# Kernel tuning notes

Measured on AMD Instinct MI355X. Metric: run time of the kernel, lower is better.

Reference implementation:

```python
import jax, jax.numpy as jnp
import numpy as np

L, B, N, D, H, DH, M = 2, 8, 1024, 256, 4, 64, 512
EPS = 1e-5


def setup_inputs() -> dict:
    key = jax.random.key(0)
    ks = jax.random.split(key, 24)
    n = lambda k, shape, s=0.02: jax.random.normal(k, shape, dtype=jnp.float32) * s
    return {
        "x": jax.random.normal(ks[0], (B, N, D), dtype=jnp.float32),
        "ln1_g": jnp.ones((L, D), jnp.float32), "ln1_b": jnp.zeros((L, D), jnp.float32),
        "w_qkv": n(ks[1], (L, D, 3 * H * DH)),
        "w_out": n(ks[2], (L, H * DH, D)), "b_out": jnp.zeros((L, D), jnp.float32),
        "ln2_g": jnp.ones((L, D), jnp.float32), "ln2_b": jnp.zeros((L, D), jnp.float32),
        "w_fc1": n(ks[3], (L, D, M)), "b_fc1": jnp.zeros((L, M), jnp.float32),
        "wh": n(ks[4], (L, M, 3), 0.3), "bh": jnp.zeros((L, M), jnp.float32),
        "wv": n(ks[5], (L, M, 3), 0.3), "bv": jnp.zeros((L, M), jnp.float32),
        "bn_g": jnp.ones((L, M), jnp.float32), "bn_b": jnp.zeros((L, M), jnp.float32),
        "bn_m": n(ks[6], (L, M), 0.1),
        "bn_v": jax.random.uniform(ks[7], (L, M), jnp.float32, 0.5, 1.5),
        "w_fc2": n(ks[8], (L, M, D)), "b_fc2": jnp.zeros((L, D), jnp.float32),
        "ls_w1": n(ks[9], (L, D, D // 4)), "ls_w2": n(ks[10], (L, D // 4, D)),
    }


def _ln(z, g, b):
    mu = z.mean(-1, keepdims=True)
    var = ((z - mu) ** 2).mean(-1, keepdims=True)
    return (z - mu) / jnp.sqrt(var + EPS) * g + b


def _lsrc(z, w1, w2):
    # SE gate: global mean over tokens -> FC -> ReLU -> FC -> sigmoid -> scale
    s = jax.nn.sigmoid(jax.nn.relu(z.mean(1) @ w1) @ w2)  # [B, D]
    return z * s[:, None, :]


def reference(x, ln1_g, ln1_b, w_qkv, w_out, b_out, ln2_g, ln2_b, w_fc1, b_fc1,
              wh, bh, wv, bv, bn_g, bn_b, bn_m, bn_v, w_fc2, b_fc2, ls_w1, ls_w2):
    scale = DH ** -0.5
    for l in range(L):
        # --- MHSA (pre-LN) ---
        h = _ln(x, ln1_g[l], ln1_b[l])
        qkv = h @ w_qkv[l]                                  # [B,N,3*H*DH]
        q, k, v = jnp.split(qkv, 3, axis=-1)
        split = lambda t: t.reshape(B, N, H, DH).transpose(0, 2, 1, 3)  # [B,H,N,DH]
        q, k, v = split(q), split(k), split(v)
        attn = jax.nn.softmax(jnp.einsum('bhid,bhjd->bhij', q, k) * scale, axis=-1)
        o = jnp.einsum('bhij,bhjd->bhid', attn, v)
        o = o.transpose(0, 2, 1, 3).reshape(B, N, H * DH)
        y = o @ w_out[l] + b_out[l]                          # dropout = identity (eval)
        x = _lsrc(x + y, ls_w1[l], ls_w2[l])
        # --- MLP with ACB depthwise conv over the token axis ---
        y = jax.nn.gelu(_ln(x, ln2_g[l], ln2_b[l]) @ w_fc1[l] + b_fc1[l], approximate=False)
        # conv_h: depthwise 1x3 conv along N (zero pad)
        yp = jnp.pad(y, ((0, 0), (1, 1), (0, 0)))
        ch = wh[l, :, 0] * yp[:, :-2] + wh[l, :, 1] * yp[:, 1:-1] + wh[l, :, 2] * yp[:, 2:] + bh[l]
        # conv_v: 3x1 depthwise conv on height-1 input with pad 1 -> only center tap
        cv = wv[l, :, 1] * y + bv[l]
        z = ch + cv
        z = (z - bn_m[l]) / jnp.sqrt(bn_v[l] + EPS) * bn_g[l] + bn_b[l]  # BN (eval)
        z = jax.nn.gelu(z, approximate=False)
        y = z @ w_fc2[l] + b_fc2[l]
        x = _lsrc(x + y, ls_w1[l], ls_w2[l])
    return x
```

## Files before the change

kernel.cpp:

```cpp
#include <hip/hip_runtime.h>
#include <hip/hip_bf16.h>
#include <math.h>

#define EPSF 1e-5f

typedef short bf16x8 __attribute__((ext_vector_type(8)));
typedef float f32x4  __attribute__((ext_vector_type(4)));

#define S_BARRIER   __asm__ volatile("s_barrier" ::: "memory")
#define S_WAITV(n)  __asm__ volatile("s_waitcnt vmcnt(" #n ")" ::: "memory")
#define S_WAITL0    __asm__ volatile("s_waitcnt lgkmcnt(0)" ::: "memory")

__device__ __forceinline__ float gelu_f(float z){
  return 0.5f*z*(1.0f + erff(z*0.70710678118654752f));
}
__device__ __forceinline__ unsigned short f2bf(float f){
  unsigned u = __float_as_uint(f);
  u += 0x7FFFu + ((u >> 16) & 1u);
  return (unsigned short)(u >> 16);
}
__device__ __forceinline__ float bf2f(unsigned short u){
  return __uint_as_float((unsigned)u << 16);
}
__device__ __forceinline__ void gll16(const unsigned short* g, unsigned short* l){
  __builtin_amdgcn_global_load_lds(
    (const __attribute__((address_space(1))) unsigned int*)g,
    (__attribute__((address_space(3))) unsigned int*)l, 16, 0, 0);
}

__global__ void tcast_all_k(const float* __restrict__ wqkv, const float* __restrict__ wout,
                            const float* __restrict__ wfc1, const float* __restrict__ wfc2,
                            unsigned short* __restrict__ oqkv, unsigned short* __restrict__ oout,
                            unsigned short* __restrict__ ofc1, unsigned short* __restrict__ ofc2,
                            const float* __restrict__ wh, const float* __restrict__ bh,
                            const float* __restrict__ wv, const float* __restrict__ bv,
                            const float* __restrict__ g, const float* __restrict__ bb,
                            const float* __restrict__ mm, const float* __restrict__ vv,
                            float* __restrict__ cp){
  int idx = blockIdx.x*256 + threadIdx.x;
  if (idx < 1048576){
    int l = idx >> 19; int r = idx & 524287;
    const float* in; unsigned short* out; int K, N, base;
    if (r < 196608)      { in=wqkv+ (long)l*196608; out=oqkv+(long)l*196608; K=256; N=768; base=r; }
    else if (r < 262144) { in=wout+ (long)l*65536;  out=oout+(long)l*65536;  K=256; N=256; base=r-196608; }
    else if (r < 393216) { in=wfc1+ (long)l*131072; out=ofc1+(long)l*131072; K=256; N=512; base=r-262144; }
    else                 { in=wfc2+ (long)l*131072; out=ofc2+(long)l*131072; K=512; N=256; base=r-393216; }
    int n = base / K, k = base % K;
    out[base] = f2bf(in[(long)k*N + n]);
  } else if (idx < 1048576 + 1024){
    int j2 = idx - 1048576;
    int l = j2 >> 9, j = j2 & 511;
    int o = l*512 + j;
    float sc = g[o]*rsqrtf(vv[o] + EPSF);
    float* c = cp + (long)l*6*512;
    c[0*512+j] = wh[o*3+0];
    c[1*512+j] = wh[o*3+1] + wv[o*3+1];
    c[2*512+j] = wh[o*3+2];
    c[3*512+j] = bh[o] + bv[o];
    c[4*512+j] = sc;
    c[5*512+j] = bb[o] - mm[o]*sc;
  }
}

__global__ void ln_bf_k(const float* __restrict__ x, const float* __restrict__ g,
                        const float* __restrict__ b, unsigned short* __restrict__ out){
  const int wv = threadIdx.x >> 6, lane = threadIdx.x & 63;
  const int row = blockIdx.x*4 + wv;
  const int c4 = lane*4;
  float4 v = *reinterpret_cast<const float4*>(x + (long)row*256 + c4);
  float s  = v.x+v.y+v.z+v.w;
  float s2 = v.x*v.x+v.y*v.y+v.z*v.z+v.w*v.w;
  #pragma unroll
  for (int o=32;o>0;o>>=1){ s += __shfl_xor(s,o); s2 += __shfl_xor(s2,o); }
  const float mu = s*(1.f/256.f);
  const float rstd = rsqrtf(s2*(1.f/256.f) - mu*mu + EPSF);
  float4 gg = *reinterpret_cast<const float4*>(g + c4);
  float4 bb = *reinterpret_cast<const float4*>(b + c4);
  ushort4 u;
  u.x = f2bf((v.x-mu)*rstd*gg.x + bb.x);
  u.y = f2bf((v.y-mu)*rstd*gg.y + bb.y);
  u.z = f2bf((v.z-mu)*rstd*gg.z + bb.z);
  u.w = f2bf((v.w-mu)*rstd*gg.w + bb.w);
  *reinterpret_cast<ushort4*>(out + (long)row*256 + c4) = u;
}

__global__ void seapply_ln_k(float* __restrict__ x, const float* __restrict__ gate,
                             const float* __restrict__ g, const float* __restrict__ b,
                             unsigned short* __restrict__ out){
  const int wv = threadIdx.x >> 6, lane = threadIdx.x & 63;
  const int row = blockIdx.x*4 + wv;
  const int bi = row >> 10;
  const int c4 = lane*4;
  float4 v = *reinterpret_cast<const float4*>(x + (long)row*256 + c4);
  float4 gt = *reinterpret_cast<const float4*>(gate + bi*256 + c4);
  v.x*=gt.x; v.y*=gt.y; v.z*=gt.z; v.w*=gt.w;
  *reinterpret_cast<float4*>(x + (long)row*256 + c4) = v;
  float s  = v.x+v.y+v.z+v.w;
  float s2 = v.x*v.x+v.y*v.y+v.z*v.z+v.w*v.w;
  #pragma unroll
  for (int o=32;o>0;o>>=1){ s += __shfl_xor(s,o); s2 += __shfl_xor(s2,o); }
  const float mu = s*(1.f/256.f);
  const float rstd = rsqrtf(s2*(1.f/256.f) - mu*mu + EPSF);
  float4 gg = *reinterpret_cast<const float4*>(g + c4);
  float4 bb = *reinterpret_cast<const float4*>(b + c4);
  ushort4 u;
  u.x = f2bf((v.x-mu)*rstd*gg.x + bb.x);
  u.y = f2bf((v.y-mu)*rstd*gg.y + bb.y);
  u.z = f2bf((v.z-mu)*rstd*gg.z + bb.z);
  u.w = f2bf((v.w-mu)*rstd*gg.w + bb.w);
  *reinterpret_cast<ushort4*>(out + (long)row*256 + c4) = u;
}

__global__ void seapply_out_k(const float* __restrict__ x, const float* __restrict__ gate,
                              float* __restrict__ o){
  long o4 = ((long)blockIdx.x*256 + threadIdx.x)*4;
  float4 v = *reinterpret_cast<const float4*>(x+o4);
  float4 g = *reinterpret_cast<const float4*>(gate + (((o4>>18)<<8) | (o4 & 255)));
  v.x*=g.x; v.y*=g.y; v.z*=g.z; v.w*=g.w;
  *reinterpret_cast<float4*>(o+o4) = v;
}

template<int ACT, bool RES, bool BIAS, int OUT, int BMT, int BNT, bool CS>
__global__ __launch_bounds__(256,2)
void gmm_k(const unsigned short* __restrict__ A,
           const unsigned short* __restrict__ Bt,
           void* __restrict__ Cv, int ldc,
           const float* __restrict__ bias,
           const float* __restrict__ res,
           int K, unsigned short* __restrict__ vtb,
           float* __restrict__ cm)
{
  __shared__ unsigned short As[2][BMT*64];
  __shared__ unsigned short Bs[2][BNT*64];
  float* C = (float*)Cv;
  unsigned short* Cb = (unsigned short*)Cv;
  const int tid  = threadIdx.x;
  const int wave = tid>>6, lane = tid&63;
  constexpr int NI = BMT/32;
  constexpr int NJ = BNT/32;
  constexpr int NDMA = BMT/32 + BNT/32;
  const int wm = (wave>>1)*(16*NI), wn = (wave&1)*(BNT/2);
  const int m0 = blockIdx.y*BMT, n0 = blockIdx.x*BNT;
  const int lrow = lane&15, quad = lane>>4;

  f32x4 acc[NI][NJ];
  #pragma unroll
  for (int i=0;i<NI;i++)
    #pragma unroll
    for (int j=0;j<NJ;j++)
      #pragma unroll
      for (int r=0;r<4;r++) acc[i][j][r]=0.f;

  auto stage = [&](int kt, int buf){
    const int k0 = kt<<6;
    #pragma unroll
    for (int it2=0; it2<BMT/32; it2++){
      int idx = tid + it2*256;
      int row = idx>>3, c = idx&7;
      gll16(A + (long)(m0+row)*K + k0 + c*8, &As[buf][idx*8]);
    }
    #pragma unroll
    for (int it2=0; it2<BNT/32; it2++){
      int idx = tid + it2*256;
      int row = idx>>3, c = idx&7;
      gll16(Bt + (long)(n0+row)*K + k0 + c*8, &Bs[buf][idx*8]);
    }
  };

  const int iters = K >> 6;
  stage(0, 0);

  for (int it=0; it<iters; it++){
    const int cur = it & 1;
    if (it+1 < iters){
      stage(it+1, cur^1);
      if constexpr (NDMA==8) { S_WAITV(8); }
      else if constexpr (NDMA==6) { S_WAITV(6); }
      else { S_WAITV(4); }
    } else {
      S_WAITV(0);
    }
    S_BARRIER;

    #pragma unroll
    for (int s=0;s<2;s++){
      bf16x8 a[NI], b[NJ];
      const int ck = s*4 + quad;
      #pragma unroll
      for (int i=0;i<NI;i++)
        a[i] = *reinterpret_cast<const bf16x8*>(&As[cur][(wm+16*i+lrow)*64 + ck*8]);
      #pragma unroll
      for (int j=0;j<NJ;j++)
        b[j] = *reinterpret_cast<const bf16x8*>(&Bs[cur][(wn+16*j+lrow)*64 + ck*8]);
      #pragma unroll
      for (int i=0;i<NI;i++)
        #pragma unroll
        for (int j=0;j<NJ;j++)
          acc[i][j] = __builtin_amdgcn_mfma_f32_16x16x32_bf16(a[i], b[j], acc[i][j], 0,0,0);
    }
    S_WAITL0;
    S_BARRIER;
  }

  if constexpr (OUT==2){
    if (n0 >= 512){
      unsigned short* lt = (unsigned short*)&As[0][0];
      #pragma unroll
      for (int i=0;i<NI;i++){
        const int row_l0 = wm + 16*i + quad*4;
        #pragma unroll
        for (int j=0;j<NJ;j++){
          const int col_l = wn + 16*j + lrow;
          #pragma unroll
          for (int r=0;r<4;r++){
            const int row_l = row_l0 + r;
            lt[col_l*128 + (((row_l>>3) ^ (col_l&7))<<3) + (row_l&7)] = f2bf(acc[i][j][r]);
          }
        }
      }
      __syncthreads();
      const int bb = m0 >> 10, nn0 = m0 & 1023;
      #pragma unroll
      for (int it2=0; it2<8; it2++){
        int idx = tid + it2*256;
        int col_l = idx >> 4;
        int row8 = (idx & 15) << 3;
        uint4 v = *reinterpret_cast<const uint4*>(&lt[col_l*128 + (((row8>>3) ^ (col_l&7))<<3)]);
        int col = n0 + col_l;
        int h = (col-512) >> 6, d = (col-512) & 63;
        *reinterpret_cast<uint4*>(&vtb[(long)((bb*4+h)*64 + d)*1024 + nn0 + row8]) = v;
      }
      return;
    }
    #pragma unroll
    for (int i=0;i<NI;i++){
      const int row0 = m0 + wm + 16*i + quad*4;
      #pragma unroll
      for (int j=0;j<NJ;j++){
        const int col = n0 + wn + 16*j + lrow;
        #pragma unroll
        for (int r=0;r<4;r++)
          Cb[(long)(row0+r)*512 + col] = f2bf(acc[i][j][r]);
      }
    }
    return;
  }

  float csum[NJ];
  #pragma unroll
  for (int j=0;j<NJ;j++) csum[j] = 0.f;

  #pragma unroll
  for (int i=0;i<NI;i++){
    const int row0 = m0 + wm + 16*i + quad*4;
    #pragma unroll
    for (int j=0;j<NJ;j++){
      const int col = n0 + wn + 16*j + lrow;
      const float bv = BIAS ? bias[col] : 0.f;
      #pragma unroll
      for (int r=0;r<4;r++){
        const long off = (long)(row0+r)*ldc + col;
        float v = acc[i][j][r] + bv;
        if (RES) v += res[off];
        if (ACT==1) v = gelu_f(v);
        if (CS) csum[j] += v;
        if (OUT==1) Cb[off] = f2bf(v); else C[off] = v;
      }
    }
  }
  if (CS){
    float* red = (float*)&As[0][0];
    for (int j = tid; j < BNT; j += 256) red[j] = 0.f;
    __syncthreads();
    #pragma unroll
    for (int j=0;j<NJ;j++)
      atomicAdd(&red[wn + 16*j + lrow], csum[j]);
    __syncthreads();
    const int bb = m0 >> 10;
    for (int j = tid; j < BNT; j += 256)
      atomicAdd(&cm[bb*256 + n0 + j], red[j]);
  }
}

__global__ __launch_bounds__(256)
void attn_k(const unsigned short* __restrict__ qkb,
            const unsigned short* __restrict__ vtb,
            unsigned short* __restrict__ op, float* __restrict__ ml){
  const int q0 = blockIdx.x * 64;
  const int bh = blockIdx.y;
  const int kz = blockIdx.z;
  const int b = bh >> 2, h = bh & 3;
  const int tid = threadIdx.x;
  const int wv = tid >> 6;
  const int lane = tid & 63;
  const int l15 = lane & 15, quad = lane >> 4;

  __shared__ unsigned short Qs[64*64];
  __shared__ unsigned short Ks[64*64];
  __shared__ unsigned short Vt[64*64];
  __shared__ unsigned short Ps[64*64];

  const long rowbase = (long)b*1024;
  const unsigned short* vsrc = vtb + (long)bh*64*1024;

  for (int f = tid; f < 512; f += 256){
    int row = f >> 3, g = f & 7;
    *reinterpret_cast<uint4*>(&Qs[row*64 + (g ^ (row&7))*8]) =
      *reinterpret_cast<const uint4*>(qkb + (rowbase + q0 + row)*512 + h*64 + g*8);
  }

  const int row0 = tid >> 3, g0 = tid & 7;
  const int row1 = row0 + 32;
  uint4 kr0, vr0, kr1, vr1;
  auto pre = [&](int k0){
    kr0 = *reinterpret_cast<const uint4*>(qkb + (rowbase + k0 + row0)*512 + 256 + h*64 + g0*8);
    vr0 = *reinterpret_cast<const uint4*>(vsrc + (long)row0*1024 + k0 + g0*8);
    kr1 = *reinterpret_cast<const uint4*>(qkb + (rowbase + k0 + row1)*512 + 256 + h*64 + g0*8);
    vr1 = *reinterpret_cast<const uint4*>(vsrc + (long)row1*1024 + k0 + g0*8);
  };

  float lp[4];
  f32x4 acc[4];
  #pragma unroll
  for (int r=0;r<4;r++) lp[r] = 0.f;
  #pragma unroll
  for (int j=0;j<4;j++)
    #pragma unroll
    for (int r=0;r<4;r++) acc[j][r] = 0.f;

  const int kbeg = kz*512, kend = kbeg + 512;
  pre(kbeg);
  for (int k0 = kbeg; k0 < kend; k0 += 64){
    *reinterpret_cast<uint4*>(&Ks[row0*64 + (g0 ^ (row0&7))*8]) = kr0;
    *reinterpret_cast<uint4*>(&Vt[row0*64 + (g0 ^ (row0&7))*8]) = vr0;
    *reinterpret_cast<uint4*>(&Ks[row1*64 + (g0 ^ (row1&7))*8]) = kr1;
    *reinterpret_cast<uint4*>(&Vt[row1*64 + (g0 ^ (row1&7))*8]) = vr1;
    __syncthreads();
    if (k0 + 64 < kend) pre(k0 + 64);

    f32x4 s[4];
    #pragma unroll
    for (int j=0;j<4;j++)
      #pragma unroll
      for (int r=0;r<4;r++) s[j][r] = 0.f;

    #pragma unroll
    for (int half=0; half<2; half++){
      const int ck = half*4 + quad;
      const int qrow = 16*wv + l15;
      bf16x8 a = *reinterpret_cast<const bf16x8*>(&Qs[qrow*64 + (ck ^ (qrow&7))*8]);
      #pragma unroll
      for (int j=0;j<4;j++){
        int krow = 16*j + l15;
        bf16x8 bb = *reinterpret_cast<const bf16x8*>(&Ks[krow*64 + (ck ^ (krow&7))*8]);
        s[j] = __builtin_amdgcn_mfma_f32_16x16x32_bf16(a, bb, s[j], 0,0,0);
      }
    }

    #pragma unroll
    for (int r=0;r<4;r++)
      #pragma unroll
      for (int j=0;j<4;j++){
        float p = __expf(s[j][r]*0.125f);
        s[j][r] = p;
        lp[r] += p;
      }

    #pragma unroll
    for (int j=0;j<4;j++)
      #pragma unroll
      for (int r=0;r<4;r++){
        int rowq = 16*wv + quad*4 + r;
        int key = l15 + 16*j;
        Ps[rowq*64 + (((key>>3) ^ ((rowq>>2)&7)))*8 + (key&7)] = f2bf(s[j][r]);
      }

    #pragma unroll
    for (int half=0; half<2; half++){
      const int ck = half*4 + quad;
      const int prow = 16*wv + l15;
      bf16x8 a = *reinterpret_cast<const bf16x8*>(&Ps[prow*64 + (ck ^ ((prow>>2)&7))*8]);
      #pragma unroll
      for (int jj=0;jj<4;jj++){
        int drow = 16*jj + l15;
        bf16x8 bb = *reinterpret_cast<const bf16x8*>(&Vt[drow*64 + (ck ^ (drow&7))*8]);
        acc[jj] = __builtin_amdgcn_mfma_f32_16x16x32_bf16(a, bb, acc[jj], 0,0,0);
      }
    }
    __syncthreads();
  }

  #pragma unroll
  for (int r=0;r<4;r++){
    float l = lp[r];
    l += __shfl_xor(l, 1); l += __shfl_xor(l, 2);
    l += __shfl_xor(l, 4); l += __shfl_xor(l, 8);
    const int rloc = q0 + 16*wv + quad*4 + r;
    const long grow = rowbase + rloc;
    #pragma unroll
    for (int jj=0;jj<4;jj++)
      op[((long)kz*8192 + grow)*256 + h*64 + 16*jj + l15] = f2bf(acc[jj][r]);
    if (l15 == 0)
      ml[((long)kz*32 + bh)*1024 + rloc] = l;
  }
}

__global__ void attn_merge_k(const unsigned short* __restrict__ op, const float* __restrict__ ml,
                             unsigned short* __restrict__ o, float* __restrict__ cm){
  if (blockIdx.x == 0){
    for (int i = threadIdx.x; i < 2048; i += 256) cm[i] = 0.f;
  }
  long off = ((long)blockIdx.x*256 + threadIdx.x)*4;
  int row = (int)(off >> 8);
  int col = (int)(off & 255);
  int h = col >> 6;
  int b = row >> 10, n = row & 1023;
  int bh = b*4 + h;
  float l0 = ml[(long)bh*1024 + n];
  float l1 = ml[32768 + (long)bh*1024 + n];
  float inv = 1.f / (l0 + l1);
  ushort4 a0 = *reinterpret_cast<const ushort4*>(op + off);
  ushort4 a1 = *reinterpret_cast<const ushort4*>(op + 2097152 + off);
  ushort4 u;
  u.x = f2bf((bf2f(a0.x) + bf2f(a1.x))*inv);
  u.y = f2bf((bf2f(a0.y) + bf2f(a1.y))*inv);
  u.z = f2bf((bf2f(a0.z) + bf2f(a1.z))*inv);
  u.w = f2bf((bf2f(a0.w) + bf2f(a1.w))*inv);
  *reinterpret_cast<ushort4*>(o + off) = u;
}

__global__ void segate2_k(const float* __restrict__ cm, const float* __restrict__ w1,
                          const float* __restrict__ w2, float* __restrict__ gate){
  const int b = blockIdx.x, t = threadIdx.x;
  __shared__ float sc[256], sh[64];
  sc[t] = cm[b*256+t]*(1.f/1024.f);
  __syncthreads();
  if (t < 64){
    float a=0.f;
    for (int k=0;k<256;k++) a += sc[k]*w1[k*64+t];
    sh[t] = fmaxf(a, 0.f);
  }
  __syncthreads();
  float a=0.f;
  for (int k=0;k<64;k++) a += sh[k]*w2[k*256+t];
  gate[b*256+t] = 1.f/(1.f+__expf(-a));
}

__global__ void conv_bf_k(const unsigned short* __restrict__ y, unsigned short* __restrict__ z,
                          const float* __restrict__ cp, float* __restrict__ cm)
{
  if (blockIdx.x == 0){
    for (int i = threadIdx.x; i < 2048; i += 256) cm[i] = 0.f;
  }
  const int t = threadIdx.x;
  const int rr = t >> 6;
  const int row = blockIdx.x*4 + rr;
  const int n = row & 1023;
  const int c8 = (t & 63) * 8;
  const long base = (long)row*512 + c8;

  uint4 uc = *reinterpret_cast<const uint4*>(y + base);
  uint4 um = (n>0)    ? *reinterpret_cast<const uint4*>(y + base - 512) : uint4{0,0,0,0};
  uint4 up = (n<1023) ? *reinterpret_cast<const uint4*>(y + base + 512) : uint4{0,0,0,0};
  const unsigned short* yc = reinterpret_cast<const unsigned short*>(&uc);
  const unsigned short* ym = reinterpret_cast<const unsigned short*>(&um);
  const unsigned short* yp = reinterpret_cast<const unsigned short*>(&up);

  float c0[8], c1[8], c2[8], c3[8], s5[8], b5[8];
  #pragma unroll
  for (int q=0;q<8;q+=4){
    *reinterpret_cast<float4*>(&c0[q]) = *reinterpret_cast<const float4*>(cp + 0*512 + c8 + q);
    *reinterpret_cast<float4*>(&c1[q]) = *reinterpret_cast<const float4*>(cp + 1*512 + c8 + q);
    *reinterpret_cast<float4*>(&c2[q]) = *reinterpret_cast<const float4*>(cp + 2*512 + c8 + q);
    *reinterpret_cast<float4*>(&c3[q]) = *reinterpret_cast<const float4*>(cp + 3*512 + c8 + q);
    *reinterpret_cast<float4*>(&s5[q]) = *reinterpret_cast<const float4*>(cp + 4*512 + c8 + q);
    *reinterpret_cast<float4*>(&b5[q]) = *reinterpret_cast<const float4*>(cp + 5*512 + c8 + q);
  }

  unsigned short outv[8];
  #pragma unroll
  for (int q=0;q<8;q++){
    float zz = c0[q]*bf2f(ym[q]) + c1[q]*bf2f(yc[q]) + c2[q]*bf2f(yp[q]) + c3[q];
    zz = zz*s5[q] + b5[q];
    outv[q] = f2bf(gelu_f(zz));
  }
  *reinterpret_cast<uint4*>(z + base) = *reinterpret_cast<uint4*>(outv);
}

extern "C" void kernel_launch(void* const* d_in, const int* in_sizes, int n_in,
                              void* d_out, int out_size, void* d_ws, size_t ws_size,
                              hipStream_t stream)
{
  const float* x_in  = (const float*)d_in[0];
  const float* ln1_g = (const float*)d_in[1];
  const float* ln1_b = (const float*)d_in[2];
  const float* w_qkv = (const float*)d_in[3];
  const float* w_out = (const float*)d_in[4];
  const float* b_out = (const float*)d_in[5];
  const float* ln2_g = (const float*)d_in[6];
  const float* ln2_b = (const float*)d_in[7];
  const float* w_fc1 = (const float*)d_in[8];
  const float* b_fc1 = (const float*)d_in[9];
  const float* wh    = (const float*)d_in[10];
  const float* bh    = (const float*)d_in[11];
  const float* wv    = (const float*)d_in[12];
  const float* bv    = (const float*)d_in[13];
  const float* bn_g  = (const float*)d_in[14];
  const float* bn_b  = (const float*)d_in[15];
  const float* bn_m  = (const float*)d_in[16];
  const float* bn_v  = (const float*)d_in[17];
  const float* w_fc2 = (const float*)d_in[18];
  const float* b_fc2 = (const float*)d_in[19];
  const float* ls_w1 = (const float*)d_in[20];
  const float* ls_w2 = (const float*)d_in[21];

  float* ws   = (float*)d_ws;
  float* xbuf = ws;
  float* mlb  = xbuf + 2097152;
  float* cm   = mlb + 65536;
  float* gate = cm + 2048;
  float* cpar = gate + 2048;
  unsigned short* habf = (unsigned short*)(cpar + 6144);
  unsigned short* opbf = habf + 2097152;
  unsigned short* qkb  = opbf + 4194304;
  unsigned short* vtb  = qkb  + 4194304;
  unsigned short* ybf  = vtb  + 2097152;
  unsigned short* zbf  = ybf  + 4194304;
  unsigned short* wqkv_t = zbf + 4194304;
  unsigned short* wout_t = wqkv_t + 393216;
  unsigned short* wfc1_t = wout_t + 131072;
  unsigned short* wfc2_t = wfc1_t + 262144;

  tcast_all_k<<<4100,256,0,stream>>>(w_qkv, w_out, w_fc1, w_fc2,
                                     wqkv_t, wout_t, wfc1_t, wfc2_t,
                                     wh, bh, wv, bv, bn_g, bn_b, bn_m, bn_v, cpar);

  for (int l=0;l<2;l++){
    const float* bout_l = b_out + l*256;
    const float* bfc1_l = b_fc1 + l*512;
    const float* bfc2_l = b_fc2 + l*256;
    const float* lw1_l  = ls_w1 + (long)l*256*64;
    const float* lw2_l  = ls_w2 + (long)l*64*256;
    const float* resx   = (l==0) ? x_in : xbuf;

    if (l==0)
      ln_bf_k<<<2048,256,0,stream>>>(x_in, ln1_g, ln1_b, habf);
    gmm_k<0,false,false,2,128,128,false><<<dim3(6,64),256,0,stream>>>(
        habf, wqkv_t + (long)l*768*256, (void*)qkb, 512, nullptr, nullptr, 256, vtb, nullptr);
    attn_k<<<dim3(16,32,2),256,0,stream>>>(qkb, vtb, opbf, mlb);
    attn_merge_k<<<2048,256,0,stream>>>(opbf, mlb, habf, cm);
    gmm_k<0,true,true,0,64,64,true><<<dim3(4,128),256,0,stream>>>(
        habf, wout_t + (long)l*256*256, (void*)xbuf, 256, bout_l, resx, 256, nullptr, cm);

    segate2_k<<<8,256,0,stream>>>(cm, lw1_l, lw2_l, gate);
    seapply_ln_k<<<2048,256,0,stream>>>(xbuf, gate, ln2_g + l*256, ln2_b + l*256, habf);

    gmm_k<1,false,true,1,128,128,false><<<dim3(4,64),256,0,stream>>>(
        habf, wfc1_t + (long)l*512*256, (void*)ybf, 512, bfc1_l, nullptr, 256, nullptr, nullptr);
    conv_bf_k<<<2048,256,0,stream>>>(ybf, zbf, cpar + (long)l*6*512, cm);
    gmm_k<0,true,true,0,64,64,true><<<dim3(4,128),256,0,stream>>>(
        zbf, wfc2_t + (long)l*256*512, (void*)xbuf, 256, bfc2_l, xbuf, 512, nullptr, cm);

    segate2_k<<<8,256,0,stream>>>(cm, lw1_l, lw2_l, gate);
    if (l==0)
      seapply_ln_k<<<2048,256,0,stream>>>(xbuf, gate, ln1_g + 256, ln1_b + 256, habf);
    else
      seapply_out_k<<<2048,256,0,stream>>>(xbuf, gate, (float*)d_out);
  }
}
```

Baseline: 318.4 us.

## Drop attention KV split and merge kernel, tile weight transpose, move colsum zeroing

Attention now processes the full 1024-key range in one block and normalizes in place, which removes the split-K partial outputs and the separate merge kernel. That saves one launch and the extra global traffic for the partials, but halves the attention grid to 512 blocks. The weight transpose-cast now goes through a shared-memory tile with coalesced reads and vector writes instead of strided scalar accesses. Zeroing of the column-sum buffer moves into the setup kernel and into segate2_k, and segate2_k's first FC is split across all 256 threads.

Measured after the change: 317.5 us. About the same (-0.3%).

```diff
diff --git a/kernel.cpp b/kernel.cpp
--- a/kernel.cpp
+++ b/kernel.cpp
@@ -36,21 +36,35 @@
                             const float* __restrict__ wv, const float* __restrict__ bv,
                             const float* __restrict__ g, const float* __restrict__ bb,
                             const float* __restrict__ mm, const float* __restrict__ vv,
-                            float* __restrict__ cp){
-  int idx = blockIdx.x*256 + threadIdx.x;
-  if (idx < 1048576){
-    int l = idx >> 19; int r = idx & 524287;
-    const float* in; unsigned short* out; int K, N, base;
-    if (r < 196608)      { in=wqkv+ (long)l*196608; out=oqkv+(long)l*196608; K=256; N=768; base=r; }
-    else if (r < 262144) { in=wout+ (long)l*65536;  out=oout+(long)l*65536;  K=256; N=256; base=r-196608; }
-    else if (r < 393216) { in=wfc1+ (long)l*131072; out=ofc1+(long)l*131072; K=256; N=512; base=r-262144; }
-    else                 { in=wfc2+ (long)l*131072; out=ofc2+(long)l*131072; K=512; N=256; base=r-393216; }
-    int n = base / K, k = base % K;
-    out[base] = f2bf(in[(long)k*N + n]);
-  } else if (idx < 1048576 + 1024){
-    int j2 = idx - 1048576;
-    int l = j2 >> 9, j = j2 & 511;
-    int o = l*512 + j;
+                            float* __restrict__ cp, float* __restrict__ cm){
+  const int b = blockIdx.x, t = threadIdx.x;
+  if (b < 256){
+    __shared__ unsigned short lt[64*68];
+    const int l = b >> 7, r = b & 127;
+    const float* in; unsigned short* out; int K, N, tk, tn;
+    if (r < 48)      { in=wqkv+(long)l*196608; out=oqkv+(long)l*196608; K=256; N=768; tk=r&3;          tn=r>>2; }
+    else if (r < 64) { int q=r-48; in=wout+(long)l*65536;  out=oout+(long)l*65536;  K=256; N=256; tk=q&3; tn=q>>2; }
+    else if (r < 96) { int q=r-64; in=wfc1+(long)l*131072; out=ofc1+(long)l*131072; K=256; N=512; tk=q&3; tn=q>>2; }
+    else             { int q=r-96; in=wfc2+(long)l*131072; out=ofc2+(long)l*131072; K=512; N=256; tk=q&7; tn=q>>3; }
+    const int k0 = tk<<6, n0 = tn<<6;
+    const int nn = t & 63, kq = t >> 6;
+    #pragma unroll
+    for (int i=0;i<16;i++){
+      const int kl = kq*16 + i;
+      lt[nn*68 + kl] = f2bf(in[(long)(k0+kl)*N + n0 + nn]);
+    }
+    __syncthreads();
+    const int k4 = (t & 15) << 2;
+    #pragma unroll
+    for (int p=0;p<4;p++){
+      const int nl = p*16 + (t>>4);
+      *reinterpret_cast<ushort4*>(&out[(long)(n0+nl)*K + k0 + k4]) =
+        *reinterpret_cast<const ushort4*>(&lt[nl*68 + k4]);
+    }
+  } else if (b < 260){
+    const int j2 = (b-256)*256 + t;
+    const int l = j2 >> 9, j = j2 & 511;
+    const int o = l*512 + j;
     float sc = g[o]*rsqrtf(vv[o] + EPSF);
     float* c = cp + (long)l*6*512;
     c[0*512+j] = wh[o*3+0];
@@ -59,6 +73,8 @@
     c[3*512+j] = bh[o] + bv[o];
     c[4*512+j] = sc;
     c[5*512+j] = bb[o] - mm[o]*sc;
+  } else {
+    cm[(b-260)*256 + t] = 0.f;
   }
 }
 
@@ -285,10 +301,9 @@
 __global__ __launch_bounds__(256)
 void attn_k(const unsigned short* __restrict__ qkb,
             const unsigned short* __restrict__ vtb,
-            unsigned short* __restrict__ op, float* __restrict__ ml){
+            unsigned short* __restrict__ o){
   const int q0 = blockIdx.x * 64;
   const int bh = blockIdx.y;
-  const int kz = blockIdx.z;
   const int b = bh >> 2, h = bh & 3;
   const int tid = threadIdx.x;
   const int wv = tid >> 6;
@@ -328,15 +343,14 @@
     #pragma unroll
     for (int r=0;r<4;r++) acc[j][r] = 0.f;
 
-  const int kbeg = kz*512, kend = kbeg + 512;
-  pre(kbeg);
-  for (int k0 = kbeg; k0 < kend; k0 += 64){
+  pre(0);
+  for (int k0 = 0; k0 < 1024; k0 += 64){
     *reinterpret_cast<uint4*>(&Ks[row0*64 + (g0 ^ (row0&7))*8]) = kr0;
     *reinterpret_cast<uint4*>(&Vt[row0*64 + (g0 ^ (row0&7))*8]) = vr0;
     *reinterpret_cast<uint4*>(&Ks[row1*64 + (g0 ^ (row1&7))*8]) = kr1;
     *reinterpret_cast<uint4*>(&Vt[row1*64 + (g0 ^ (row1&7))*8]) = vr1;
     __syncthreads();
-    if (k0 + 64 < kend) pre(k0 + 64);
+    if (k0 + 64 < 1024) pre(k0 + 64);
 
     f32x4 s[4];
     #pragma unroll
@@ -395,63 +409,44 @@
     float l = lp[r];
     l += __shfl_xor(l, 1); l += __shfl_xor(l, 2);
     l += __shfl_xor(l, 4); l += __shfl_xor(l, 8);
+    const float inv = 1.f / l;
     const int rloc = q0 + 16*wv + quad*4 + r;
     const long grow = rowbase + rloc;
     #pragma unroll
     for (int jj=0;jj<4;jj++)
-      op[((long)kz*8192 + grow)*256 + h*64 + 16*jj + l15] = f2bf(acc[jj][r]);
-    if (l15 == 0)
-      ml[((long)kz*32 + bh)*1024 + rloc] = l;
-  }
-}
-
-__global__ void attn_merge_k(const unsigned short* __restrict__ op, const float* __restrict__ ml,
-                             unsigned short* __restrict__ o, float* __restrict__ cm){
-  if (blockIdx.x == 0){
-    for (int i = threadIdx.x; i < 2048; i += 256) cm[i] = 0.f;
-  }
-  long off = ((long)blockIdx.x*256 + threadIdx.x)*4;
-  int row = (int)(off >> 8);
-  int col = (int)(off & 255);
-  int h = col >> 6;
-  int b = row >> 10, n = row & 1023;
-  int bh = b*4 + h;
-  float l0 = ml[(long)bh*1024 + n];
-  float l1 = ml[32768 + (long)bh*1024 + n];
-  float inv = 1.f / (l0 + l1);
-  ushort4 a0 = *reinterpret_cast<const ushort4*>(op + off);
-  ushort4 a1 = *reinterpret_cast<const ushort4*>(op + 2097152 + off);
-  ushort4 u;
-  u.x = f2bf((bf2f(a0.x) + bf2f(a1.x))*inv);
-  u.y = f2bf((bf2f(a0.y) + bf2f(a1.y))*inv);
-  u.z = f2bf((bf2f(a0.z) + bf2f(a1.z))*inv);
-  u.w = f2bf((bf2f(a0.w) + bf2f(a1.w))*inv);
-  *reinterpret_cast<ushort4*>(o + off) = u;
-}
-
-__global__ void segate2_k(const float* __restrict__ cm, const float* __restrict__ w1,
+      o[grow*256 + h*64 + 16*jj + l15] = f2bf(acc[jj][r]*inv);
+  }
+}
+
+__global__ void segate2_k(float* __restrict__ cm, const float* __restrict__ w1,
                           const float* __restrict__ w2, float* __restrict__ gate){
   const int b = blockIdx.x, t = threadIdx.x;
   __shared__ float sc[256], sh[64];
   sc[t] = cm[b*256+t]*(1.f/1024.f);
+  cm[b*256+t] = 0.f;
   __syncthreads();
-  if (t < 64){
-    float a=0.f;
-    for (int k=0;k<256;k++) a += sc[k]*w1[k*64+t];
-    sh[t] = fmaxf(a, 0.f);
+  {
+    const int j = t >> 2, part = t & 3;
+    float a = 0.f;
+    #pragma unroll 4
+    for (int i=0;i<64;i++){
+      const int k = i*4 + part;
+      a += sc[k]*w1[k*64+j];
+    }
+    a += __shfl_xor(a, 1);
+    a += __shfl_xor(a, 2);
+    if (part == 0) sh[j] = fmaxf(a, 0.f);
   }
   __syncthreads();
-  float a=0.f;
+  float a = 0.f;
+  #pragma unroll 8
   for (int k=0;k<64;k++) a += sh[k]*w2[k*256+t];
   gate[b*256+t] = 1.f/(1.f+__expf(-a));
 }
 
 __global__ void conv_bf_k(const unsigned short* __restrict__ y, unsigned short* __restrict__ z,
-                          const float* __restrict__ cp, float* __restrict__ cm)
+                          const float* __restrict__ cp)
 {
-  if (blockIdx.x == 0){
-    for (int i = threadIdx.x; i < 2048; i += 256) cm[i] = 0.f;
-  }
   const int t = threadIdx.x;
   const int rr = t >> 6;
   const int row = blockIdx.x*4 + rr;
@@ -516,13 +511,11 @@
 
   float* ws   = (float*)d_ws;
   float* xbuf = ws;
-  float* mlb  = xbuf + 2097152;
-  float* cm   = mlb + 65536;
+  float* cm   = xbuf + 2097152;
   float* gate = cm + 2048;
   float* cpar = gate + 2048;
   unsigned short* habf = (unsigned short*)(cpar + 6144);
-  unsigned short* opbf = habf + 2097152;
-  unsigned short* qkb  = opbf + 4194304;
+  unsigned short* qkb  = habf + 2097152;
   unsigned short* vtb  = qkb  + 4194304;
   unsigned short* ybf  = vtb  + 2097152;
   unsigned short* zbf  = ybf  + 4194304;
@@ -531,9 +524,9 @@
   unsigned short* wfc1_t = wout_t + 131072;
   unsigned short* wfc2_t = wfc1_t + 262144;
 
-  tcast_all_k<<<4100,256,0,stream>>>(w_qkv, w_out, w_fc1, w_fc2,
-                                     wqkv_t, wout_t, wfc1_t, wfc2_t,
-                                     wh, bh, wv, bv, bn_g, bn_b, bn_m, bn_v, cpar);
+  tcast_all_k<<<268,256,0,stream>>>(w_qkv, w_out, w_fc1, w_fc2,
+                                    wqkv_t, wout_t, wfc1_t, wfc2_t,
+                                    wh, bh, wv, bv, bn_g, bn_b, bn_m, bn_v, cpar, cm);
 
   for (int l=0;l<2;l++){
     const float* bout_l = b_out + l*256;
@@ -547,8 +540,7 @@
       ln_bf_k<<<2048,256,0,stream>>>(x_in, ln1_g, ln1_b, habf);
     gmm_k<0,false,false,2,128,128,false><<<dim3(6,64),256,0,stream>>>(
         habf, wqkv_t + (long)l*768*256, (void*)qkb, 512, nullptr, nullptr, 256, vtb, nullptr);
-    attn_k<<<dim3(16,32,2),256,0,stream>>>(qkb, vtb, opbf, mlb);
-    attn_merge_k<<<2048,256,0,stream>>>(opbf, mlb, habf, cm);
+    attn_k<<<dim3(16,32),256,0,stream>>>(qkb, vtb, habf);
     gmm_k<0,true,true,0,64,64,true><<<dim3(4,128),256,0,stream>>>(
         habf, wout_t + (long)l*256*256, (void*)xbuf, 256, bout_l, resx, 256, nullptr, cm);
 
@@ -557,7 +549,7 @@
 
     gmm_k<1,false,true,1,128,128,false><<<dim3(4,64),256,0,stream>>>(
         habf, wfc1_t + (long)l*512*256, (void*)ybf, 512, bfc1_l, nullptr, 256, nullptr, nullptr);
-    conv_bf_k<<<2048,256,0,stream>>>(ybf, zbf, cpar + (long)l*6*512, cm);
+    conv_bf_k<<<2048,256,0,stream>>>(ybf, zbf, cpar + (long)l*6*512);
     gmm_k<0,true,true,0,64,64,true><<<dim3(4,128),256,0,stream>>>(
         zbf, wfc2_t + (long)l*256*512, (void*)xbuf, 256, bfc2_l, xbuf, 512, nullptr, cm);
 
```
